# Kernel tuning notes

Measured on AMD Instinct MI355X. Metric: run time of the kernel, lower is better.

Reference implementation:

```python
import jax, jax.numpy as jnp
import numpy as np

N = 100000   # nodes
E = 3200000  # edges (avg degree 32)
F = 10       # input features
H = 20       # hidden dim
G = 512      # graphs in batch
L = 2        # labels


def xavier(key, shape):
    fan_in, fan_out = shape[0], shape[1]
    a = jnp.sqrt(6.0 / (fan_in + fan_out))
    return jax.random.uniform(key, shape, jnp.float32, -a, a)


def setup_inputs() -> dict:
    key = jax.random.key(0)
    ks = jax.random.split(key, 12)
    x = jax.random.normal(ks[0], (N, F), jnp.float32)
    edge_index = jax.random.randint(ks[1], (2, E), 0, N, jnp.int64)
    batch = jnp.sort(jax.random.randint(ks[2], (N,), 0, G, jnp.int64))
    return {
        "x": x,
        "edge_index": edge_index,
        "batch": batch,
        # layer 1: F -> H
        "W_rel1": xavier(ks[3], (F, H)), "b1": jnp.zeros((H,), jnp.float32),
        "W_root1": xavier(ks[4], (F, H)),
        # layer 2: H -> H
        "W_rel2": xavier(ks[5], (H, H)), "b2": jnp.zeros((H,), jnp.float32),
        "W_root2": xavier(ks[6], (H, H)),
        # layer 3: H -> H
        "W_rel3": xavier(ks[7], (H, H)), "b3": jnp.zeros((H,), jnp.float32),
        "W_root3": xavier(ks[8], (H, H)),
        # readout linear: 2H -> L
        "W_lin": xavier(ks[9], (2 * H, L)), "b_lin": jnp.zeros((L,), jnp.float32),
    }


def _graph_conv(x, src, dst, W_rel, b, W_root):
    # PyG GraphConv: out = lin_rel(sum_{j->i} x_j) + lin_root(x_i)
    agg = jax.ops.segment_sum(x[src], dst, num_segments=N)  # [N, d_in]
    return agg @ W_rel + b + x @ W_root


def reference(x, edge_index, batch, W_rel1, b1, W_root1, W_rel2, b2, W_root2,
              W_rel3, b3, W_root3, W_lin, b_lin):
    src, dst = edge_index[0], edge_index[1]
    h = jax.nn.relu(_graph_conv(x, src, dst, W_rel1, b1, W_root1))
    h = jax.nn.relu(_graph_conv(h, src, dst, W_rel2, b2, W_root2))
    h = jax.nn.relu(_graph_conv(h, src, dst, W_rel3, b3, W_root3))  # [N, H]
    # global max / mean pool over graphs
    maxp = jax.ops.segment_max(h, batch, num_segments=G)            # [G, H]
    sump = jax.ops.segment_sum(h, batch, num_segments=G)            # [G, H]
    counts = jax.ops.segment_sum(jnp.ones((h.shape[0], 1), h.dtype), batch,
                                 num_segments=G)                    # [G, 1]
    nonempty = counts > 0
    maxp = jnp.where(nonempty, maxp, 0.0)
    meanp = sump / jnp.maximum(counts, 1.0)
    pooled = jnp.concatenate([maxp, meanp], axis=-1)                # [G, 2H]
    return pooled @ W_lin + b_lin
```

## Files before the change

kernel.cpp:

```cpp
#include <hip/hip_runtime.h>
#include <hip/hip_bf16.h>

#define NN 100000
#define FF 10
#define HH 20
#define GG 512
#define LL 2

#define NB 500
#define BNODES 200
#define CAP 7168
#define HB 100
#define SCAP 3712
#define TILE 4096
#define SRC_BITS 17
#define SRC_MASK 0x1FFFFu

__device__ inline unsigned short f2bf(float f) {
  unsigned u = __float_as_uint(f);
  unsigned r = u + 0x7FFFu + ((u >> 16) & 1u);
  return (unsigned short)(r >> 16);
}
__device__ inline float bflo(unsigned u) { return __uint_as_float(u << 16); }
__device__ inline float bfhi(unsigned u) { return __uint_as_float(u & 0xFFFF0000u); }

__global__ __launch_bounds__(256) void cast_init_kernel(
    const float* __restrict__ x, unsigned short* __restrict__ xb,
    float* __restrict__ sump, int* __restrict__ maxp, float* __restrict__ cnt,
    int* __restrict__ cursor, int n) {
  int i = blockIdx.x * 256 + threadIdx.x;
  if (i < n) xb[i] = f2bf(__builtin_nontemporal_load(x + i));
  if (i < GG * HH) {
    sump[i] = 0.0f;
    maxp[i] = 0;
  }
  if (i < GG) cnt[i] = 0.0f;
  if (i < NB) cursor[i] = 0;
}

__global__ __launch_bounds__(512) void multisplit_kernel(
    const int* __restrict__ src, const int* __restrict__ dst,
    int* __restrict__ cursor, unsigned int* __restrict__ pay, int E) {
  __shared__ int lhist[NB];
  __shared__ int lofs[NB];
  __shared__ int gbase[NB];
  __shared__ int lcur[NB];
  __shared__ unsigned int sord[TILE];
  __shared__ unsigned short sdbk[TILE];
  __shared__ int ss[512];
  int t = threadIdx.x;
  if (t < NB) lhist[t] = 0;
  __syncthreads();

  int base = blockIdx.x * TILE;
  int count = E - base;
  if (count > TILE) count = TILE;

  for (int i = t; i < count; i += 512)
    atomicAdd(&lhist[dst[base + i] / BNODES], 1);
  __syncthreads();

  int own = (t < NB) ? lhist[t] : 0;
  ss[t] = own;
  __syncthreads();
  for (int off = 1; off < 512; off <<= 1) {
    int a0 = (t >= off) ? ss[t - off] : 0;
    __syncthreads();
    ss[t] += a0;
    __syncthreads();
  }
  if (t < NB) {
    lofs[t] = ss[t] - own;
    int bo = own ? atomicAdd(&cursor[t], own) : 0;
    if (bo > CAP - own) bo = CAP - own;
    gbase[t] = t * CAP + bo;
    lcur[t] = 0;
  }
  __syncthreads();

  for (int i = t; i < count; i += 512) {
    int e = base + i;
    int d = __builtin_nontemporal_load(dst + e);
    int s = __builtin_nontemporal_load(src + e);
    int bk = d / BNODES;
    int ld = d - bk * BNODES;
    int r = atomicAdd(&lcur[bk], 1);
    int slot = lofs[bk] + r;
    sord[slot] = ((unsigned)ld << SRC_BITS) | (unsigned)s;
    sdbk[slot] = (unsigned short)bk;
  }
  __syncthreads();

  for (int i = t; i < count; i += 512) {
    int bk = sdbk[i];
    pay[gbase[bk] + (i - lofs[bk])] = sord[i];
  }
}

template<int DIN>
__global__ __launch_bounds__(512) void bucket_layer_kernel(
    const unsigned short* __restrict__ hin, const unsigned int* __restrict__ pay,
    const int* __restrict__ cursor, const float* __restrict__ Wrel,
    const float* __restrict__ bias, const float* __restrict__ Wroot,
    unsigned short* __restrict__ hout) {
  constexpr int AST = (DIN == 10) ? 11 : 21;
  constexpr int CH = DIN / 5;
  __shared__ int sSrc[SCAP];
  __shared__ float acc[HB * AST];
  __shared__ unsigned short roots[HB * DIN];
  __shared__ float sWrel[DIN * HH];
  __shared__ float sWroot[DIN * HH];
  __shared__ float sb[HH];
  __shared__ int lhist[HB];
  __shared__ int lcur[HB];
  __shared__ int sRofs[HB];
  __shared__ int sRend[HB];
  __shared__ int ss[128];
  int b2 = blockIdx.x;
  int bucket = b2 >> 1;
  int lo = (b2 & 1) * HB;
  int t = threadIdx.x;
  int nbase = b2 * HB;

  for (int i = t; i < DIN * HH; i += 512) {
    sWrel[i] = Wrel[i];
    sWroot[i] = Wroot[i];
  }
  if (t < HH) sb[t] = bias[t];
  if (t < HB) lhist[t] = 0;
  {
    const unsigned* rs = (const unsigned*)(hin + (size_t)nbase * DIN);
    unsigned* rd = (unsigned*)roots;
    for (int i = t; i < HB * DIN / 2; i += 512) rd[i] = rs[i];
  }
  __syncthreads();

  int ecnt = cursor[bucket];
  if (ecnt > CAP) ecnt = CAP;
  const unsigned int* mypay = pay + (size_t)bucket * CAP;

  for (int i = t; i < ecnt; i += 512) {
    int ld = (int)(__builtin_nontemporal_load(mypay + i) >> SRC_BITS) - lo;
    if ((unsigned)ld < HB) atomicAdd(&lhist[ld], 1);
  }
  __syncthreads();

  int own = (t < HB) ? lhist[t] : 0;
  if (t < 128) ss[t] = own;
  __syncthreads();
  for (int off = 1; off < 128; off <<= 1) {
    int a0 = (t < 128 && t >= off) ? ss[t - off] : 0;
    __syncthreads();
    if (t < 128) ss[t] += a0;
    __syncthreads();
  }
  if (t < HB) {
    int ex = ss[t] - own;
    sRofs[t] = ex;
    int en = ex + own;
    sRend[t] = en < SCAP ? en : SCAP;
    lcur[t] = 0;
  }
  __syncthreads();

  for (int i = t; i < ecnt; i += 512) {
    unsigned p = __builtin_nontemporal_load(mypay + i);
    int ld = (int)(p >> SRC_BITS) - lo;
    if ((unsigned)ld < HB) {
      int r = atomicAdd(&lcur[ld], 1);
      int slot = sRofs[ld] + r;
      if (slot < SCAP) sSrc[slot] = (int)(p & SRC_MASK);
    }
  }
  __syncthreads();

  if (t < HB * 5) {
    int ln = t / 5;
    int c = t - ln * 5;
    int k0 = sRofs[ln], k1 = sRend[ln];
    float a0 = 0, a1 = 0, a2 = 0, a3 = 0;
    const unsigned short* xb = hin + c * CH;
    if (CH == 4) {
      for (int k = k0; k < k1; k++) {
        uint2 u = *(const uint2*)(xb + (size_t)sSrc[k] * DIN);
        a0 += bflo(u.x);
        a1 += bfhi(u.x);
        a2 += bflo(u.y);
        a3 += bfhi(u.y);
      }
    } else {
      for (int k = k0; k < k1; k++) {
        unsigned u = *(const unsigned*)(xb + (size_t)sSrc[k] * DIN);
        a0 += bflo(u);
        a1 += bfhi(u);
      }
    }
    float* a = acc + ln * AST + c * CH;
    if (CH == 4) {
      a[0] = a0; a[1] = a1; a[2] = a2; a[3] = a3;
    } else {
      a[0] = a0; a[1] = a1;
    }
  }
  __syncthreads();

  for (int idx = t; idx < HB * HH; idx += 512) {
    int ln = idx / HH;
    int j = idx - ln * HH;
    const float* a = acc + ln * AST;
    const unsigned short* r = roots + ln * DIN;
    float v = sb[j];
#pragma unroll
    for (int f = 0; f < DIN; f++) {
      v += a[f] * sWrel[f * HH + j];
      v += bflo((unsigned)r[f]) * sWroot[f * HH + j];
    }
    hout[(size_t)nbase * HH + idx] = f2bf(fmaxf(v, 0.0f));
  }
}

__global__ __launch_bounds__(512) void bucket_layer_pool_kernel(
    const unsigned short* __restrict__ hin, const unsigned int* __restrict__ pay,
    const int* __restrict__ cursor, const float* __restrict__ Wrel,
    const float* __restrict__ bias, const float* __restrict__ Wroot,
    const int* __restrict__ batch, float* __restrict__ sump,
    int* __restrict__ maxp, float* __restrict__ cnt) {
  constexpr int DIN = 20;
  constexpr int AST = 21;
  __shared__ int sSrc[SCAP];
  __shared__ float acc[HB * AST];
  __shared__ unsigned short roots[HB * DIN];
  __shared__ int sBatch[HB];
  __shared__ float sWrel[DIN * HH];
  __shared__ float sWroot[DIN * HH];
  __shared__ float sb[HH];
  __shared__ int lhist[HB];
  __shared__ int lcur[HB];
  __shared__ int sRofs[HB];
  __shared__ int sRend[HB];
  __shared__ int ss[128];
  int b2 = blockIdx.x;
  int bucket = b2 >> 1;
  int lo = (b2 & 1) * HB;
  int t = threadIdx.x;
  int nbase = b2 * HB;

  for (int i = t; i < DIN * HH; i += 512) {
    sWrel[i] = Wrel[i];
    sWroot[i] = Wroot[i];
  }
  if (t < HH) sb[t] = bias[t];
  if (t < HB) {
    lhist[t] = 0;
    sBatch[t] = batch[nbase + t];
  }
  {
    const unsigned* rs = (const unsigned*)(hin + (size_t)nbase * DIN);
    unsigned* rd = (unsigned*)roots;
    for (int i = t; i < HB * DIN / 2; i += 512) rd[i] = rs[i];
  }
  __syncthreads();

  int ecnt = cursor[bucket];
  if (ecnt > CAP) ecnt = CAP;
  const unsigned int* mypay = pay + (size_t)bucket * CAP;

  for (int i = t; i < ecnt; i += 512) {
    int ld = (int)(__builtin_nontemporal_load(mypay + i) >> SRC_BITS) - lo;
    if ((unsigned)ld < HB) atomicAdd(&lhist[ld], 1);
  }
  __syncthreads();

  int own = (t < HB) ? lhist[t] : 0;
  if (t < 128) ss[t] = own;
  __syncthreads();
  for (int off = 1; off < 128; off <<= 1) {
    int a0 = (t < 128 && t >= off) ? ss[t - off] : 0;
    __syncthreads();
    if (t < 128) ss[t] += a0;
    __syncthreads();
  }
  if (t < HB) {
    int ex = ss[t] - own;
    sRofs[t] = ex;
    int en = ex + own;
    sRend[t] = en < SCAP ? en : SCAP;
    lcur[t] = 0;
  }
  __syncthreads();

  for (int i = t; i < ecnt; i += 512) {
    unsigned p = __builtin_nontemporal_load(mypay + i);
    int ld = (int)(p >> SRC_BITS) - lo;
    if ((unsigned)ld < HB) {
      int r = atomicAdd(&lcur[ld], 1);
      int slot = sRofs[ld] + r;
      if (slot < SCAP) sSrc[slot] = (int)(p & SRC_MASK);
    }
  }
  __syncthreads();

  if (t < HB * 5) {
    int ln = t / 5;
    int c = t - ln * 5;
    int k0 = sRofs[ln], k1 = sRend[ln];
    float a0 = 0, a1 = 0, a2 = 0, a3 = 0;
    const unsigned short* xb = hin + c * 4;
    for (int k = k0; k < k1; k++) {
      uint2 u = *(const uint2*)(xb + (size_t)sSrc[k] * 20);
      a0 += bflo(u.x);
      a1 += bfhi(u.x);
      a2 += bflo(u.y);
      a3 += bfhi(u.y);
    }
    float* a = acc + ln * AST + c * 4;
    a[0] = a0; a[1] = a1; a[2] = a2; a[3] = a3;
  }
  __syncthreads();

  float vreg[4];
#pragma unroll
  for (int u = 0; u < 4; u++) {
    int idx = t + u * 512;
    if (idx < HB * HH) {
      int ln = idx / HH;
      int j = idx - ln * HH;
      const float* a = acc + ln * AST;
      const unsigned short* r = roots + ln * DIN;
      float v = sb[j];
#pragma unroll
      for (int f = 0; f < DIN; f++) {
        v += a[f] * sWrel[f * HH + j];
        v += bflo((unsigned)r[f]) * sWroot[f * HH + j];
      }
      vreg[u] = fmaxf(v, 0.0f);
    }
  }
  __syncthreads();
#pragma unroll
  for (int u = 0; u < 4; u++) {
    int idx = t + u * 512;
    if (idx < HB * HH) {
      int ln = idx / HH;
      int j = idx - ln * HH;
      acc[ln * AST + j] = vreg[u];
    }
  }
  __syncthreads();

  int g0 = sBatch[0];
  int g1 = sBatch[HB - 1];
  int ngr = g1 - g0 + 1;
  for (int it = t; it < ngr * HH; it += 512) {
    int gi = it / HH;
    int j = it - gi * HH;
    int g = g0 + gi;
    float s = 0.0f, m = 0.0f;
    int c = 0;
    for (int ln = 0; ln < HB; ln++) {
      if (sBatch[ln] == g) {
        float v = acc[ln * AST + j];
        s += v;
        m = fmaxf(m, v);
        c++;
      }
    }
    if (c) {
      atomicAdd(&sump[g * HH + j], s);
      atomicMax(&maxp[g * HH + j], __float_as_int(m));
      if (j == 0) atomicAdd(&cnt[g], (float)c);
    }
  }
}

__global__ __launch_bounds__(256) void readout_kernel(
    const float* __restrict__ sump, const int* __restrict__ maxp,
    const float* __restrict__ cnt, const float* __restrict__ Wlin,
    const float* __restrict__ blin, float* __restrict__ out) {
  int idx = blockIdx.x * 256 + threadIdx.x;
  if (idx >= GG * LL) return;
  int g = idx / LL;
  int l = idx - g * LL;
  float c = cnt[g];
  float inv = 1.0f / fmaxf(c, 1.0f);
  float acc = blin[l];
#pragma unroll
  for (int j = 0; j < HH; j++) {
    float mx = __int_as_float(maxp[g * HH + j]);
    float mean = sump[g * HH + j] * inv;
    acc += mx * Wlin[j * LL + l];
    acc += mean * Wlin[(HH + j) * LL + l];
  }
  out[idx] = acc;
}

extern "C" void kernel_launch(void* const* d_in, const int* in_sizes, int n_in,
                              void* d_out, int out_size, void* d_ws,
                              size_t ws_size, hipStream_t stream) {
  const float* x = (const float*)d_in[0];
  const int* edge_index = (const int*)d_in[1];
  const int* batch = (const int*)d_in[2];
  const float* W_rel1 = (const float*)d_in[3];
  const float* b1 = (const float*)d_in[4];
  const float* W_root1 = (const float*)d_in[5];
  const float* W_rel2 = (const float*)d_in[6];
  const float* b2 = (const float*)d_in[7];
  const float* W_root2 = (const float*)d_in[8];
  const float* W_rel3 = (const float*)d_in[9];
  const float* b3 = (const float*)d_in[10];
  const float* W_root3 = (const float*)d_in[11];
  const float* W_lin = (const float*)d_in[12];
  const float* b_lin = (const float*)d_in[13];
  float* out = (float*)d_out;

  const int E = in_sizes[1] / 2;
  const int n_nodes = in_sizes[0] / FF;
  const int* src = edge_index;
  const int* dst = edge_index + E;

  unsigned int* pay = (unsigned int*)d_ws;
  int* cursor = (int*)(pay + (size_t)NB * CAP);
  float* sump = (float*)(cursor + 512);
  int* maxp = (int*)(sump + GG * HH);
  float* cnt = (float*)(maxp + GG * HH);
  unsigned short* xb = (unsigned short*)(cnt + 512);
  unsigned short* h1 = xb + (size_t)NN * FF;
  unsigned short* h2 = h1 + (size_t)NN * HH;

  const int edge_tiles = (E + TILE - 1) / TILE;

  cast_init_kernel<<<(n_nodes * FF + 255) / 256, 256, 0, stream>>>(
      x, xb, sump, maxp, cnt, cursor, n_nodes * FF);

  multisplit_kernel<<<edge_tiles, 512, 0, stream>>>(src, dst, cursor, pay, E);

  bucket_layer_kernel<FF><<<NB * 2, 512, 0, stream>>>(
      xb, pay, cursor, W_rel1, b1, W_root1, h1);
  bucket_layer_kernel<HH><<<NB * 2, 512, 0, stream>>>(
      h1, pay, cursor, W_rel2, b2, W_root2, h2);
  bucket_layer_pool_kernel<<<NB * 2, 512, 0, stream>>>(
      h2, pay, cursor, W_rel3, b3, W_root3, batch, sump, maxp, cnt);

  readout_kernel<<<(GG * LL + 255) / 256, 256, 0, stream>>>(
      sump, maxp, cnt, W_lin, b_lin, out);
}
```

Measured before the change: 290.2 us.

## Build per-bucket CSR once and reuse it across all three layers

Adds a bucket_csr_kernel that turns each bucket's payload into a node-sorted CSR (source indices plus per-node offsets). This happens once instead of redoing the histogram, scan and scatter inside every layer kernel. Each layer kernel now reads its half-bucket segment of sorted sources straight into shared memory. The cost is an extra kernel launch, an extra global write and read of the sorted array, and more workspace memory.

Result: faster. 261.6 us (-9.9%).

```diff
diff --git a/kernel.cpp b/kernel.cpp
--- a/kernel.cpp
+++ b/kernel.cpp
@@ -97,12 +97,57 @@
   }
 }
 
+__global__ __launch_bounds__(256) void bucket_csr_kernel(
+    const unsigned int* __restrict__ pay, const int* __restrict__ cursor,
+    int* __restrict__ srt, int* __restrict__ rofs, int* __restrict__ rend) {
+  __shared__ int lhist[BNODES];
+  __shared__ int lofs[BNODES];
+  __shared__ int lcur[BNODES];
+  __shared__ int ss[256];
+  int b = blockIdx.x;
+  int t = threadIdx.x;
+  int k0 = b * CAP;
+  int ecnt = cursor[b];
+  if (ecnt > CAP) ecnt = CAP;
+
+  if (t < BNODES) lhist[t] = 0;
+  __syncthreads();
+  for (int k = t; k < ecnt; k += 256)
+    atomicAdd(&lhist[pay[k0 + k] >> SRC_BITS], 1);
+  __syncthreads();
+
+  int own = (t < BNODES) ? lhist[t] : 0;
+  ss[t] = own;
+  __syncthreads();
+  for (int off = 1; off < 256; off <<= 1) {
+    int a0 = (t >= off) ? ss[t - off] : 0;
+    __syncthreads();
+    ss[t] += a0;
+    __syncthreads();
+  }
+  if (t < BNODES) {
+    int ex = ss[t] - own;
+    lofs[t] = ex;
+    lcur[t] = 0;
+    rofs[b * BNODES + t] = k0 + ex;
+    rend[b * BNODES + t] = k0 + ex + own;
+  }
+  __syncthreads();
+
+  for (int k = t; k < ecnt; k += 256) {
+    unsigned p = pay[k0 + k];
+    int ld = p >> SRC_BITS;
+    int r = atomicAdd(&lcur[ld], 1);
+    srt[k0 + lofs[ld] + r] = (int)(p & SRC_MASK);
+  }
+}
+
 template<int DIN>
 __global__ __launch_bounds__(512) void bucket_layer_kernel(
-    const unsigned short* __restrict__ hin, const unsigned int* __restrict__ pay,
-    const int* __restrict__ cursor, const float* __restrict__ Wrel,
-    const float* __restrict__ bias, const float* __restrict__ Wroot,
-    unsigned short* __restrict__ hout) {
+    const unsigned short* __restrict__ hin, const int* __restrict__ srt,
+    const int* __restrict__ rofs, const int* __restrict__ rend,
+    const float* __restrict__ Wrel, const float* __restrict__ bias,
+    const float* __restrict__ Wroot, unsigned short* __restrict__ hout) {
   constexpr int AST = (DIN == 10) ? 11 : 21;
   constexpr int CH = DIN / 5;
   __shared__ int sSrc[SCAP];
@@ -111,14 +156,10 @@
   __shared__ float sWrel[DIN * HH];
   __shared__ float sWroot[DIN * HH];
   __shared__ float sb[HH];
-  __shared__ int lhist[HB];
-  __shared__ int lcur[HB];
   __shared__ int sRofs[HB];
   __shared__ int sRend[HB];
-  __shared__ int ss[128];
+  __shared__ int sSeg0, sSegLen;
   int b2 = blockIdx.x;
-  int bucket = b2 >> 1;
-  int lo = (b2 & 1) * HB;
   int t = threadIdx.x;
   int nbase = b2 * HB;
 
@@ -127,7 +168,16 @@
     sWroot[i] = Wroot[i];
   }
   if (t < HH) sb[t] = bias[t];
-  if (t < HB) lhist[t] = 0;
+  if (t < HB) {
+    sRofs[t] = rofs[nbase + t];
+    sRend[t] = rend[nbase + t];
+  }
+  if (t == 0) {
+    int s0 = rofs[nbase];
+    int sl = rend[nbase + HB - 1] - s0;
+    sSeg0 = s0;
+    sSegLen = sl < SCAP ? sl : SCAP;
+  }
   {
     const unsigned* rs = (const unsigned*)(hin + (size_t)nbase * DIN);
     unsigned* rd = (unsigned*)roots;
@@ -135,49 +185,16 @@
   }
   __syncthreads();
 
-  int ecnt = cursor[bucket];
-  if (ecnt > CAP) ecnt = CAP;
-  const unsigned int* mypay = pay + (size_t)bucket * CAP;
-
-  for (int i = t; i < ecnt; i += 512) {
-    int ld = (int)(__builtin_nontemporal_load(mypay + i) >> SRC_BITS) - lo;
-    if ((unsigned)ld < HB) atomicAdd(&lhist[ld], 1);
-  }
-  __syncthreads();
-
-  int own = (t < HB) ? lhist[t] : 0;
-  if (t < 128) ss[t] = own;
-  __syncthreads();
-  for (int off = 1; off < 128; off <<= 1) {
-    int a0 = (t < 128 && t >= off) ? ss[t - off] : 0;
-    __syncthreads();
-    if (t < 128) ss[t] += a0;
-    __syncthreads();
-  }
-  if (t < HB) {
-    int ex = ss[t] - own;
-    sRofs[t] = ex;
-    int en = ex + own;
-    sRend[t] = en < SCAP ? en : SCAP;
-    lcur[t] = 0;
-  }
-  __syncthreads();
-
-  for (int i = t; i < ecnt; i += 512) {
-    unsigned p = __builtin_nontemporal_load(mypay + i);
-    int ld = (int)(p >> SRC_BITS) - lo;
-    if ((unsigned)ld < HB) {
-      int r = atomicAdd(&lcur[ld], 1);
-      int slot = sRofs[ld] + r;
-      if (slot < SCAP) sSrc[slot] = (int)(p & SRC_MASK);
-    }
-  }
+  int seg0 = sSeg0, seglen = sSegLen;
+  for (int i = t; i < seglen; i += 512) sSrc[i] = srt[seg0 + i];
   __syncthreads();
 
   if (t < HB * 5) {
     int ln = t / 5;
     int c = t - ln * 5;
-    int k0 = sRofs[ln], k1 = sRend[ln];
+    int k0 = sRofs[ln] - seg0;
+    int k1 = sRend[ln] - seg0;
+    if (k1 > seglen) k1 = seglen;
     float a0 = 0, a1 = 0, a2 = 0, a3 = 0;
     const unsigned short* xb = hin + c * CH;
     if (CH == 4) {
@@ -220,11 +237,12 @@
 }
 
 __global__ __launch_bounds__(512) void bucket_layer_pool_kernel(
-    const unsigned short* __restrict__ hin, const unsigned int* __restrict__ pay,
-    const int* __restrict__ cursor, const float* __restrict__ Wrel,
-    const float* __restrict__ bias, const float* __restrict__ Wroot,
-    const int* __restrict__ batch, float* __restrict__ sump,
-    int* __restrict__ maxp, float* __restrict__ cnt) {
+    const unsigned short* __restrict__ hin, const int* __restrict__ srt,
+    const int* __restrict__ rofs, const int* __restrict__ rend,
+    const float* __restrict__ Wrel, const float* __restrict__ bias,
+    const float* __restrict__ Wroot, const int* __restrict__ batch,
+    float* __restrict__ sump, int* __restrict__ maxp,
+    float* __restrict__ cnt) {
   constexpr int DIN = 20;
   constexpr int AST = 21;
   __shared__ int sSrc[SCAP];
@@ -234,14 +252,10 @@
   __shared__ float sWrel[DIN * HH];
   __shared__ float sWroot[DIN * HH];
   __shared__ float sb[HH];
-  __shared__ int lhist[HB];
-  __shared__ int lcur[HB];
   __shared__ int sRofs[HB];
   __shared__ int sRend[HB];
-  __shared__ int ss[128];
+  __shared__ int sSeg0, sSegLen;
   int b2 = blockIdx.x;
-  int bucket = b2 >> 1;
-  int lo = (b2 & 1) * HB;
   int t = threadIdx.x;
   int nbase = b2 * HB;
 
@@ -251,8 +265,15 @@
   }
   if (t < HH) sb[t] = bias[t];
   if (t < HB) {
-    lhist[t] = 0;
+    sRofs[t] = rofs[nbase + t];
+    sRend[t] = rend[nbase + t];
     sBatch[t] = batch[nbase + t];
+  }
+  if (t == 0) {
+    int s0 = rofs[nbase];
+    int sl = rend[nbase + HB - 1] - s0;
+    sSeg0 = s0;
+    sSegLen = sl < SCAP ? sl : SCAP;
   }
   {
     const unsigned* rs = (const unsigned*)(hin + (size_t)nbase * DIN);
@@ -261,49 +282,16 @@
   }
   __syncthreads();
 
-  int ecnt = cursor[bucket];
-  if (ecnt > CAP) ecnt = CAP;
-  const unsigned int* mypay = pay + (size_t)bucket * CAP;
-
-  for (int i = t; i < ecnt; i += 512) {
-    int ld = (int)(__builtin_nontemporal_load(mypay + i) >> SRC_BITS) - lo;
-    if ((unsigned)ld < HB) atomicAdd(&lhist[ld], 1);
-  }
-  __syncthreads();
-
-  int own = (t < HB) ? lhist[t] : 0;
-  if (t < 128) ss[t] = own;
-  __syncthreads();
-  for (int off = 1; off < 128; off <<= 1) {
-    int a0 = (t < 128 && t >= off) ? ss[t - off] : 0;
-    __syncthreads();
-    if (t < 128) ss[t] += a0;
-    __syncthreads();
-  }
-  if (t < HB) {
-    int ex = ss[t] - own;
-    sRofs[t] = ex;
-    int en = ex + own;
-    sRend[t] = en < SCAP ? en : SCAP;
-    lcur[t] = 0;
-  }
-  __syncthreads();
-
-  for (int i = t; i < ecnt; i += 512) {
-    unsigned p = __builtin_nontemporal_load(mypay + i);
-    int ld = (int)(p >> SRC_BITS) - lo;
-    if ((unsigned)ld < HB) {
-      int r = atomicAdd(&lcur[ld], 1);
-      int slot = sRofs[ld] + r;
-      if (slot < SCAP) sSrc[slot] = (int)(p & SRC_MASK);
-    }
-  }
+  int seg0 = sSeg0, seglen = sSegLen;
+  for (int i = t; i < seglen; i += 512) sSrc[i] = srt[seg0 + i];
   __syncthreads();
 
   if (t < HB * 5) {
     int ln = t / 5;
     int c = t - ln * 5;
-    int k0 = sRofs[ln], k1 = sRend[ln];
+    int k0 = sRofs[ln] - seg0;
+    int k1 = sRend[ln] - seg0;
+    if (k1 > seglen) k1 = seglen;
     float a0 = 0, a1 = 0, a2 = 0, a3 = 0;
     const unsigned short* xb = hin + c * 4;
     for (int k = k0; k < k1; k++) {
@@ -419,7 +407,10 @@
   const int* dst = edge_index + E;
 
   unsigned int* pay = (unsigned int*)d_ws;
-  int* cursor = (int*)(pay + (size_t)NB * CAP);
+  int* srt = (int*)(pay + (size_t)NB * CAP);
+  int* rofs = srt + (size_t)NB * CAP;
+  int* rend = rofs + NN;
+  int* cursor = rend + NN;
   float* sump = (float*)(cursor + 512);
   int* maxp = (int*)(sump + GG * HH);
   float* cnt = (float*)(maxp + GG * HH);
@@ -433,13 +424,14 @@
       x, xb, sump, maxp, cnt, cursor, n_nodes * FF);
 
   multisplit_kernel<<<edge_tiles, 512, 0, stream>>>(src, dst, cursor, pay, E);
+  bucket_csr_kernel<<<NB, 256, 0, stream>>>(pay, cursor, srt, rofs, rend);
 
   bucket_layer_kernel<FF><<<NB * 2, 512, 0, stream>>>(
-      xb, pay, cursor, W_rel1, b1, W_root1, h1);
+      xb, srt, rofs, rend, W_rel1, b1, W_root1, h1);
   bucket_layer_kernel<HH><<<NB * 2, 512, 0, stream>>>(
-      h1, pay, cursor, W_rel2, b2, W_root2, h2);
+      h1, srt, rofs, rend, W_rel2, b2, W_root2, h2);
   bucket_layer_pool_kernel<<<NB * 2, 512, 0, stream>>>(
-      h2, pay, cursor, W_rel3, b3, W_root3, batch, sump, maxp, cnt);
+      h2, srt, rofs, rend, W_rel3, b3, W_root3, batch, sump, maxp, cnt);
 
   readout_kernel<<<(GG * LL + 255) / 256, 256, 0, stream>>>(
       sump, maxp, cnt, W_lin, b_lin, out);
```
